# Kernel tuning notes

Measured on AMD Instinct MI355X. Metric: run time of the kernel, lower is better.

Reference implementation:

```python
import jax, jax.numpy as jnp
import numpy as np

EMB_DIM = 512
LATENT_DIM = 64
D = EMB_DIM + LATENT_DIM  # 576, kernel input per side
H1, H2 = 512, 256         # MLPKernel hidden widths
B, N, M = 2, 1024, 256


def setup_inputs() -> dict:
    key = jax.random.key(0)
    ks = jax.random.split(key, 10)
    def w(k, shape, fan_in):
        return (jax.random.normal(k, shape, dtype=jnp.float32) / np.sqrt(fan_in)).astype(jnp.float32)
    return {
        "Phi_A": jax.random.normal(ks[0], (B, N, D), dtype=jnp.float32),
        "Phi_B": jax.random.normal(ks[1], (B, M, D), dtype=jnp.float32),
        # MLPKernel params: layer1 acts on concat([a,b]) (2D -> H1); split into A/B halves
        "W1a": w(ks[2], (D, H1), 2 * D),
        "W1b": w(ks[3], (D, H1), 2 * D),
        "b1": jnp.zeros((H1,), dtype=jnp.float32),
        "W2": w(ks[4], (H1, H2), H1),
        "b2": jnp.zeros((H2,), dtype=jnp.float32),
        "W3": w(ks[5], (H2, 1), H2),
        "b3": jnp.zeros((1,), dtype=jnp.float32),
    }


def reference(Phi_A, Phi_B, W1a, W1b, b1, W2, b2, W3, b3):
    # Pairwise MLP kernel: for every (n, m), MLP(concat(Phi_A[b,n], Phi_B[b,m])).
    # First layer on concat == a@W1a + b@W1b; project each side once, then broadcast-add.
    a_proj = jnp.einsum("bnd,dh->bnh", Phi_A, W1a)          # (B, N, H1)
    b_proj = jnp.einsum("bmd,dh->bmh", Phi_B, W1b)          # (B, M, H1)
    h1 = jax.nn.relu(a_proj[:, :, None, :] + b_proj[:, None, :, :] + b1)  # (B, N, M, H1)
    h2 = jax.nn.relu(jnp.einsum("bnmh,hk->bnmk", h1, W2) + b2)            # (B, N, M, H2)
    dro = jnp.einsum("bnmk,ko->bnmo", h2, W3)[..., 0] + b3[0]             # (B, N, M)
    return dro
```

## Files before the change

kernel.cpp:

```cpp
#include <hip/hip_runtime.h>

typedef float  f4  __attribute__((ext_vector_type(4)));
typedef __bf16 bf8 __attribute__((ext_vector_type(8)));

constexpr int B_ = 2, N_ = 1024, M_ = 256, D_ = 576, H1_ = 512, H2_ = 256;

__device__ __forceinline__ void gload_lds16(const void* g, void* l) {
    __builtin_amdgcn_global_load_lds((const __attribute__((address_space(1))) void*)g,
                                     (__attribute__((address_space(3))) void*)l, 16, 0, 0);
}

__global__ __launch_bounds__(256) void k_prep(
    const float* __restrict__ W1a, const float* __restrict__ W1b, const float* __restrict__ W2,
    __bf16* __restrict__ w1aT, __bf16* __restrict__ w1bT, __bf16* __restrict__ w2T) {
    __shared__ float tl[64][65];
    int bid = blockIdx.x;
    const float* src; __bf16* dst; int R, C, t0;
    if (bid < 72)       { src = W1a; dst = w1aT; R = D_;  C = H1_; t0 = bid; }
    else if (bid < 144) { src = W1b; dst = w1bT; R = D_;  C = H1_; t0 = bid - 72; }
    else                { src = W2;  dst = w2T;  R = H1_; C = H2_; t0 = bid - 144; }
    const int tilesC = C / 64;
    const int r0 = (t0 / tilesC) * 64, c0 = (t0 % tilesC) * 64;
    const int tx = threadIdx.x & 63, ty = threadIdx.x >> 6;
    #pragma unroll
    for (int i = 0; i < 16; ++i)
        tl[ty + i * 4][tx] = src[(size_t)(r0 + ty + i * 4) * C + c0 + tx];
    __syncthreads();
    #pragma unroll
    for (int i = 0; i < 16; ++i)
        dst[(size_t)(c0 + ty + i * 4) * R + r0 + tx] = (__bf16)tl[tx][ty + i * 4];
}

__global__ __launch_bounds__(512, 2) void k_proj(
    const float* __restrict__ PhiA, const float* __restrict__ PhiB,
    const __bf16* __restrict__ w1aT, const __bf16* __restrict__ w1bT,
    const float* __restrict__ b1, float* __restrict__ aproj, __bf16* __restrict__ bprojh) {
    __shared__ __bf16 as_[2][128 * 64];
    __shared__ __bf16 ws_[2][128 * 64];
    const int t = threadIdx.x, l15 = t & 15, g = (t >> 4) & 3, wid = t >> 6;
    const int wr = wid >> 2, wc = wid & 3;
    const int by = blockIdx.x, c0 = blockIdx.y * 128;
    const bool isA = (by < 16);
    const float* srcf = isA ? PhiA : PhiB;
    const int rows0 = isA ? by * 128 : (by - 16) * 128;
    const __bf16* wt = isA ? w1aT : w1bT;

    const int ra = t >> 2, kc = (t & 3) * 16;

#define STG_A(buf, kk) do {                                                       \
    const float* ap_ = srcf + (size_t)(rows0 + ra) * D_ + (kk) + kc;              \
    f4 v0_ = *(const f4*)ap_, v1_ = *(const f4*)(ap_ + 4),                        \
       v2_ = *(const f4*)(ap_ + 8), v3_ = *(const f4*)(ap_ + 12);                 \
    bf8 h0_, h1_;                                                                 \
    _Pragma("unroll")                                                             \
    for (int j_ = 0; j_ < 4; ++j_) {                                              \
        h0_[j_] = (__bf16)v0_[j_]; h0_[4 + j_] = (__bf16)v1_[j_];                 \
        h1_[j_] = (__bf16)v2_[j_]; h1_[4 + j_] = (__bf16)v3_[j_];                 \
    }                                                                             \
    *(bf8*)((char*)(&as_[(buf)][0]) + ra * 128 + ((kc * 2) ^ ((ra & 7) << 4)))      = h0_; \
    *(bf8*)((char*)(&as_[(buf)][0]) + ra * 128 + ((kc * 2 + 16) ^ ((ra & 7) << 4))) = h1_; \
    } while (0)

#define STG_W(buf, kk) do {                                                       \
    _Pragma("unroll")                                                             \
    for (int i_ = 0; i_ < 2; ++i_) {                                              \
        int c_ = t + i_ * 512; int col_ = c_ >> 3; int gg_ = (c_ & 7) ^ (col_ & 7);\
        gload_lds16(wt + (size_t)(c0 + col_) * D_ + (kk) + gg_ * 8,               \
                    (char*)(&ws_[(buf)][0]) + c_ * 16);                           \
    } } while (0)

    f4 acc[4][2];
    #pragma unroll
    for (int fr = 0; fr < 4; ++fr)
        #pragma unroll
        for (int cf = 0; cf < 2; ++cf) acc[fr][cf] = (f4)0.0f;

    STG_A(0, 0); STG_W(0, 0);
    asm volatile("s_waitcnt vmcnt(0) lgkmcnt(0)" ::: "memory");
    __builtin_amdgcn_s_barrier();
    STG_A(1, 64); STG_W(1, 64);

    #pragma unroll 1
    for (int kt = 0; kt < 9; ++kt) {
        const int cur = kt & 1;
        #pragma unroll
        for (int ks = 0; ks < 2; ++ks) {
            bf8 av[4], bv[2];
            #pragma unroll
            for (int fr = 0; fr < 4; ++fr) {
                int row = wr * 64 + fr * 16 + l15;
                av[fr] = *(const bf8*)((const char*)(&as_[cur][0]) +
                         row * 128 + ((ks * 64 + g * 16) ^ ((row & 7) << 4)));
            }
            #pragma unroll
            for (int cf = 0; cf < 2; ++cf) {
                int col = wc * 32 + cf * 16 + l15;
                bv[cf] = *(const bf8*)((const char*)(&ws_[cur][0]) +
                         col * 128 + ((ks * 64 + g * 16) ^ ((col & 7) << 4)));
            }
            #pragma unroll
            for (int fr = 0; fr < 4; ++fr)
                #pragma unroll
                for (int cf = 0; cf < 2; ++cf)
                    acc[fr][cf] = __builtin_amdgcn_mfma_f32_16x16x32_bf16(av[fr], bv[cf], acc[fr][cf], 0, 0, 0);
        }
        if (kt == 8) break;
        asm volatile("s_waitcnt vmcnt(0) lgkmcnt(0)" ::: "memory");
        __builtin_amdgcn_s_barrier();
        if (kt < 7) { STG_A(cur, (kt + 2) * 64); STG_W(cur, (kt + 2) * 64); }
    }

    #pragma unroll
    for (int fr = 0; fr < 4; ++fr)
        #pragma unroll
        for (int cf = 0; cf < 2; ++cf) {
            int col = c0 + wc * 32 + cf * 16 + l15;
            int row = rows0 + wr * 64 + fr * 16 + g * 4;
            if (isA) {
                float bb = b1[col];
                #pragma unroll
                for (int j = 0; j < 4; ++j)
                    aproj[(size_t)(row + j) * H1_ + col] = acc[fr][cf][j] + bb;
            } else {
                #pragma unroll
                for (int j = 0; j < 4; ++j)
                    bprojh[(size_t)(row + j) * H1_ + col] = (__bf16)acc[fr][cf][j];
            }
        }
#undef STG_A
#undef STG_W
}

__global__ __launch_bounds__(512, 2) void k_main(
    const float* __restrict__ aproj, const __bf16* __restrict__ bprojh,
    const __bf16* __restrict__ w2T, const float* __restrict__ b2,
    const float* __restrict__ w3, const float* __restrict__ b3,
    float* __restrict__ outp) {
    __shared__ float  apl[16 * 512];
    __shared__ __bf16 bpl[16 * 512];
    __shared__ __bf16 w2l[2][256 * 32];
    __shared__ float  part[2][256];

    const int t = threadIdx.x, l15 = t & 15, g = (t >> 4) & 3, wid = t >> 6;
    const int wr = wid >> 1, wc = wid & 1;
    const int bid = blockIdx.x;
    const int bn0 = (bid >> 4) << 4;
    const int m0 = (bid & 15) << 4;
    const int bprow0 = ((bn0 >> 10) << 8) + m0;

    int offA[4];
    #pragma unroll
    for (int fr = 0; fr < 4; ++fr) offA[fr] = (wr * 4 + fr) * 2048 + g * 32;
    int offB[8];
    #pragma unroll
    for (int cf = 0; cf < 8; ++cf) {
        int col = wc * 128 + cf * 16 + l15;
        int cp = col >> 1, sp = (((col & 1) << 2) + g) ^ (cp & 7);
        offB[cf] = cp * 128 + sp * 16;
    }
    const int offP = l15 * 1024 + (((g ^ (l15 & 3)) | (l15 & 4)) << 4);

#define STAGE_W2M(buf, ktn) do {                                                  \
    _Pragma("unroll")                                                             \
    for (int i_ = 0; i_ < 2; ++i_) {                                              \
        int c_ = t + i_ * 512; int cp_ = c_ >> 3; int sp_ = c_ & 7;               \
        int si_ = sp_ ^ (cp_ & 7); int col_ = cp_ * 2 + (si_ >> 2);               \
        gload_lds16(w2T + (size_t)col_ * H1_ + (ktn) * 32 + (si_ & 3) * 8,        \
                    (char*)w2l + (buf) * 16384 + c_ * 16);                        \
    } } while (0)

#define STAGE_AP() do {                                                           \
    _Pragma("unroll")                                                             \
    for (int i_ = 0; i_ < 4; ++i_) {                                              \
        int c_ = t + i_ * 512;                                                    \
        gload_lds16(aproj + (size_t)(bn0 + (c_ >> 7)) * H1_ + (c_ & 127) * 4,     \
                    (char*)apl + c_ * 16);                                        \
    } } while (0)

#define STAGE_BP() do {                                                           \
    _Pragma("unroll")                                                             \
    for (int i_ = 0; i_ < 2; ++i_) {                                              \
        int c_ = t + i_ * 512; int row_ = c_ >> 6; int kc_ = (c_ & 63) ^ (row_ & 7);\
        gload_lds16(bprojh + (size_t)(bprow0 + row_) * H1_ + kc_ * 8,             \
                    (char*)bpl + c_ * 16);                                        \
    } } while (0)

    f4 acc[4][8];
    #pragma unroll
    for (int fr = 0; fr < 4; ++fr)
        #pragma unroll
        for (int cf = 0; cf < 8; ++cf) acc[fr][cf] = (f4)0.0f;

    float b2v[8], w3v[8];
    #pragma unroll
    for (int cf = 0; cf < 8; ++cf) {
        int col = wc * 128 + cf * 16 + l15;
        b2v[cf] = b2[col]; w3v[cf] = w3[col];
    }

    STAGE_AP(); STAGE_BP(); STAGE_W2M(0, 0); STAGE_W2M(1, 1);
    asm volatile("s_waitcnt vmcnt(2)" ::: "memory");
    __builtin_amdgcn_s_barrier();

    #pragma unroll
    for (int kt = 0; kt < 16; ++kt) {
        const int cur = kt & 1;
        bf8 bpv = *(const bf8*)((const char*)bpl + (offP ^ (kt * 64)));
        bf8 bv[8];
        #pragma unroll
        for (int cf = 0; cf < 8; ++cf)
            bv[cf] = *(const bf8*)((const char*)w2l + offB[cf] + cur * 16384);
        f4 a0[4], a1[4];
        #pragma unroll
        for (int fr = 0; fr < 4; ++fr) {
            a0[fr] = *(const f4*)((const char*)apl + offA[fr] + kt * 128);
            a1[fr] = *(const f4*)((const char*)apl + offA[fr] + kt * 128 + 16);
        }
        float bpf[8];
        #pragma unroll
        for (int j = 0; j < 8; ++j) bpf[j] = (float)bpv[j];
        __builtin_amdgcn_s_setprio(1);
        #pragma unroll
        for (int fr = 0; fr < 4; ++fr) {
            bf8 av;
            #pragma unroll
            for (int j = 0; j < 4; ++j) {
                av[j]     = (__bf16)fmaxf(a0[fr][j] + bpf[j],     0.0f);
                av[4 + j] = (__bf16)fmaxf(a1[fr][j] + bpf[4 + j], 0.0f);
            }
            #pragma unroll
            for (int cf = 0; cf < 8; ++cf)
                acc[fr][cf] = __builtin_amdgcn_mfma_f32_16x16x32_bf16(av, bv[cf], acc[fr][cf], 0, 0, 0);
        }
        __builtin_amdgcn_s_setprio(0);
        if (kt < 15) {
            asm volatile("" ::: "memory");
            __builtin_amdgcn_s_barrier();
            if (kt < 14) STAGE_W2M(cur, kt + 2);
            if (kt < 14) asm volatile("s_waitcnt vmcnt(2)" ::: "memory");
            else         asm volatile("s_waitcnt vmcnt(0)" ::: "memory");
            __builtin_amdgcn_s_barrier();
        }
    }

    #pragma unroll
    for (int fr = 0; fr < 4; ++fr) {
        #pragma unroll
        for (int j = 0; j < 4; ++j) {
            float s = 0.0f;
            #pragma unroll
            for (int cf = 0; cf < 8; ++cf)
                s += fmaxf(acc[fr][cf][j] + b2v[cf], 0.0f) * w3v[cf];
            s += __shfl_xor(s, 1); s += __shfl_xor(s, 2);
            s += __shfl_xor(s, 4); s += __shfl_xor(s, 8);
            if (l15 == 0) part[wc][wr * 64 + fr * 16 + g * 4 + j] = s;
        }
    }
    __syncthreads();
    if (t < 256) {
        float o = part[0][t] + part[1][t] + b3[0];
        outp[(size_t)(bn0 + (t >> 4)) * M_ + m0 + (t & 15)] = o;
    }
#undef STAGE_W2M
#undef STAGE_AP
#undef STAGE_BP
}

extern "C" void kernel_launch(void* const* d_in, const int* in_sizes, int n_in,
                              void* d_out, int out_size, void* d_ws, size_t ws_size,
                              hipStream_t stream) {
    (void)in_sizes; (void)n_in; (void)out_size; (void)ws_size;
    const float* PhiA = (const float*)d_in[0];
    const float* PhiB = (const float*)d_in[1];
    const float* W1a  = (const float*)d_in[2];
    const float* W1b  = (const float*)d_in[3];
    const float* b1   = (const float*)d_in[4];
    const float* W2   = (const float*)d_in[5];
    const float* b2   = (const float*)d_in[6];
    const float* W3   = (const float*)d_in[7];
    const float* b3   = (const float*)d_in[8];
    float* out = (float*)d_out;

    char* ws = (char*)d_ws;
    float*  aproj  = (float*)(ws);
    __bf16* bprojh = (__bf16*)(ws + 4194304);
    __bf16* w1aT   = (__bf16*)(ws + 4718592);
    __bf16* w1bT   = (__bf16*)(ws + 5308416);
    __bf16* w2T    = (__bf16*)(ws + 5898240);

    k_prep<<<176, 256, 0, stream>>>(W1a, W1b, W2, w1aT, w1bT, w2T);
    k_proj<<<dim3(20, 4), 512, 0, stream>>>(PhiA, PhiB, w1aT, w1bT, b1, aproj, bprojh);
    k_main<<<2048, 512, 0, stream>>>(aproj, bprojh, w2T, b2, W3, b3, out);
}
```

Measured before the change: 250.5 us.

## Shrink main tiles, store aproj as bf16, triple-buffer W2 with single barrier

```diff
diff --git a/kernel.cpp b/kernel.cpp
--- a/kernel.cpp
+++ b/kernel.cpp
@@ -31,18 +31,18 @@
         dst[(size_t)(c0 + ty + i * 4) * R + r0 + tx] = (__bf16)tl[tx][ty + i * 4];
 }
 
-__global__ __launch_bounds__(512, 2) void k_proj(
+__global__ __launch_bounds__(256, 2) void k_proj(
     const float* __restrict__ PhiA, const float* __restrict__ PhiB,
     const __bf16* __restrict__ w1aT, const __bf16* __restrict__ w1bT,
-    const float* __restrict__ b1, float* __restrict__ aproj, __bf16* __restrict__ bprojh) {
-    __shared__ __bf16 as_[2][128 * 64];
+    const float* __restrict__ b1, __bf16* __restrict__ aprojh, __bf16* __restrict__ bprojh) {
+    __shared__ __bf16 as_[2][64 * 64];
     __shared__ __bf16 ws_[2][128 * 64];
     const int t = threadIdx.x, l15 = t & 15, g = (t >> 4) & 3, wid = t >> 6;
-    const int wr = wid >> 2, wc = wid & 3;
+    const int wr = wid >> 1, wc = wid & 1;
     const int by = blockIdx.x, c0 = blockIdx.y * 128;
-    const bool isA = (by < 16);
+    const bool isA = (by < 32);
     const float* srcf = isA ? PhiA : PhiB;
-    const int rows0 = isA ? by * 128 : (by - 16) * 128;
+    const int rows0 = isA ? by * 64 : (by - 32) * 64;
     const __bf16* wt = isA ? w1aT : w1bT;
 
     const int ra = t >> 2, kc = (t & 3) * 16;
@@ -63,17 +63,17 @@
 
 #define STG_W(buf, kk) do {                                                       \
     _Pragma("unroll")                                                             \
-    for (int i_ = 0; i_ < 2; ++i_) {                                              \
-        int c_ = t + i_ * 512; int col_ = c_ >> 3; int gg_ = (c_ & 7) ^ (col_ & 7);\
+    for (int i_ = 0; i_ < 4; ++i_) {                                              \
+        int c_ = t + i_ * 256; int col_ = c_ >> 3; int gg_ = (c_ & 7) ^ (col_ & 7);\
         gload_lds16(wt + (size_t)(c0 + col_) * D_ + (kk) + gg_ * 8,               \
                     (char*)(&ws_[(buf)][0]) + c_ * 16);                           \
     } } while (0)
 
-    f4 acc[4][2];
-    #pragma unroll
-    for (int fr = 0; fr < 4; ++fr)
-        #pragma unroll
-        for (int cf = 0; cf < 2; ++cf) acc[fr][cf] = (f4)0.0f;
+    f4 acc[2][4];
+    #pragma unroll
+    for (int fr = 0; fr < 2; ++fr)
+        #pragma unroll
+        for (int cf = 0; cf < 4; ++cf) acc[fr][cf] = (f4)0.0f;
 
     STG_A(0, 0); STG_W(0, 0);
     asm volatile("s_waitcnt vmcnt(0) lgkmcnt(0)" ::: "memory");
@@ -85,23 +85,23 @@
         const int cur = kt & 1;
         #pragma unroll
         for (int ks = 0; ks < 2; ++ks) {
-            bf8 av[4], bv[2];
-            #pragma unroll
-            for (int fr = 0; fr < 4; ++fr) {
-                int row = wr * 64 + fr * 16 + l15;
+            bf8 av[2], bv[4];
+            #pragma unroll
+            for (int fr = 0; fr < 2; ++fr) {
+                int row = wr * 32 + fr * 16 + l15;
                 av[fr] = *(const bf8*)((const char*)(&as_[cur][0]) +
                          row * 128 + ((ks * 64 + g * 16) ^ ((row & 7) << 4)));
             }
             #pragma unroll
-            for (int cf = 0; cf < 2; ++cf) {
-                int col = wc * 32 + cf * 16 + l15;
+            for (int cf = 0; cf < 4; ++cf) {
+                int col = wc * 64 + cf * 16 + l15;
                 bv[cf] = *(const bf8*)((const char*)(&ws_[cur][0]) +
                          col * 128 + ((ks * 64 + g * 16) ^ ((col & 7) << 4)));
             }
             #pragma unroll
-            for (int fr = 0; fr < 4; ++fr)
+            for (int fr = 0; fr < 2; ++fr)
                 #pragma unroll
-                for (int cf = 0; cf < 2; ++cf)
+                for (int cf = 0; cf < 4; ++cf)
                     acc[fr][cf] = __builtin_amdgcn_mfma_f32_16x16x32_bf16(av[fr], bv[cf], acc[fr][cf], 0, 0, 0);
         }
         if (kt == 8) break;
@@ -111,16 +111,16 @@
     }
 
     #pragma unroll
-    for (int fr = 0; fr < 4; ++fr)
-        #pragma unroll
-        for (int cf = 0; cf < 2; ++cf) {
-            int col = c0 + wc * 32 + cf * 16 + l15;
-            int row = rows0 + wr * 64 + fr * 16 + g * 4;
+    for (int fr = 0; fr < 2; ++fr)
+        #pragma unroll
+        for (int cf = 0; cf < 4; ++cf) {
+            int col = c0 + wc * 64 + cf * 16 + l15;
+            int row = rows0 + wr * 32 + fr * 16 + g * 4;
             if (isA) {
                 float bb = b1[col];
                 #pragma unroll
                 for (int j = 0; j < 4; ++j)
-                    aproj[(size_t)(row + j) * H1_ + col] = acc[fr][cf][j] + bb;
+                    aprojh[(size_t)(row + j) * H1_ + col] = (__bf16)(acc[fr][cf][j] + bb);
             } else {
                 #pragma unroll
                 for (int j = 0; j < 4; ++j)
@@ -131,26 +131,26 @@
 #undef STG_W
 }
 
-__global__ __launch_bounds__(512, 2) void k_main(
-    const float* __restrict__ aproj, const __bf16* __restrict__ bprojh,
+__global__ __launch_bounds__(256, 2) void k_main(
+    const __bf16* __restrict__ aprojh, const __bf16* __restrict__ bprojh,
     const __bf16* __restrict__ w2T, const float* __restrict__ b2,
     const float* __restrict__ w3, const float* __restrict__ b3,
     float* __restrict__ outp) {
-    __shared__ float  apl[16 * 512];
+    __shared__ __bf16 apl[8 * 512];
     __shared__ __bf16 bpl[16 * 512];
-    __shared__ __bf16 w2l[2][256 * 32];
-    __shared__ float  part[2][256];
+    __shared__ __bf16 w2l[3][256 * 32];
+    __shared__ float  part[2][128];
 
     const int t = threadIdx.x, l15 = t & 15, g = (t >> 4) & 3, wid = t >> 6;
     const int wr = wid >> 1, wc = wid & 1;
     const int bid = blockIdx.x;
-    const int bn0 = (bid >> 4) << 4;
-    const int m0 = (bid & 15) << 4;
+    const int bn0 = (bid >> 4) * 8;
+    const int m0 = (bid & 15) * 16;
     const int bprow0 = ((bn0 >> 10) << 8) + m0;
 
-    int offA[4];
-    #pragma unroll
-    for (int fr = 0; fr < 4; ++fr) offA[fr] = (wr * 4 + fr) * 2048 + g * 32;
+    int apA[4];
+    #pragma unroll
+    for (int fr = 0; fr < 4; ++fr) apA[fr] = (wr * 4 + fr) * 1024 + g * 16;
     int offB[8];
     #pragma unroll
     for (int cf = 0; cf < 8; ++cf) {
@@ -160,27 +160,27 @@
     }
     const int offP = l15 * 1024 + (((g ^ (l15 & 3)) | (l15 & 4)) << 4);
 
-#define STAGE_W2M(buf, ktn) do {                                                  \
-    _Pragma("unroll")                                                             \
-    for (int i_ = 0; i_ < 2; ++i_) {                                              \
-        int c_ = t + i_ * 512; int cp_ = c_ >> 3; int sp_ = c_ & 7;               \
+#define STAGE_W2M(stoff, ktn) do {                                                \
+    _Pragma("unroll")                                                             \
+    for (int i_ = 0; i_ < 4; ++i_) {                                              \
+        int c_ = t + i_ * 256; int cp_ = c_ >> 3; int sp_ = c_ & 7;               \
         int si_ = sp_ ^ (cp_ & 7); int col_ = cp_ * 2 + (si_ >> 2);               \
         gload_lds16(w2T + (size_t)col_ * H1_ + (ktn) * 32 + (si_ & 3) * 8,        \
-                    (char*)w2l + (buf) * 16384 + c_ * 16);                        \
+                    (char*)w2l + (stoff) + c_ * 16);                              \
     } } while (0)
 
 #define STAGE_AP() do {                                                           \
     _Pragma("unroll")                                                             \
+    for (int i_ = 0; i_ < 2; ++i_) {                                              \
+        int c_ = t + i_ * 256;                                                    \
+        gload_lds16(aprojh + (size_t)(bn0 + (c_ >> 6)) * H1_ + (c_ & 63) * 8,     \
+                    (char*)apl + c_ * 16);                                        \
+    } } while (0)
+
+#define STAGE_BP() do {                                                           \
+    _Pragma("unroll")                                                             \
     for (int i_ = 0; i_ < 4; ++i_) {                                              \
-        int c_ = t + i_ * 512;                                                    \
-        gload_lds16(aproj + (size_t)(bn0 + (c_ >> 7)) * H1_ + (c_ & 127) * 4,     \
-                    (char*)apl + c_ * 16);                                        \
-    } } while (0)
-
-#define STAGE_BP() do {                                                           \
-    _Pragma("unroll")                                                             \
-    for (int i_ = 0; i_ < 2; ++i_) {                                              \
-        int c_ = t + i_ * 512; int row_ = c_ >> 6; int kc_ = (c_ & 63) ^ (row_ & 7);\
+        int c_ = t + i_ * 256; int row_ = c_ >> 6; int kc_ = (c_ & 63) ^ (row_ & 7);\
         gload_lds16(bprojh + (size_t)(bprow0 + row_) * H1_ + kc_ * 8,             \
                     (char*)bpl + c_ * 16);                                        \
     } } while (0)
@@ -190,6 +190,48 @@
     for (int fr = 0; fr < 4; ++fr)
         #pragma unroll
         for (int cf = 0; cf < 8; ++cf) acc[fr][cf] = (f4)0.0f;
+
+    STAGE_AP(); STAGE_BP(); STAGE_W2M(0, 0);
+    STAGE_W2M(16384, 1);
+    asm volatile("s_waitcnt vmcnt(4)" ::: "memory");
+    __builtin_amdgcn_s_barrier();
+
+    int rdoff = 0, stoff = 32768;
+    #pragma unroll 1
+    for (int kt = 0; kt < 16; ++kt) {
+        if (kt < 14) STAGE_W2M(stoff, kt + 2);
+        const char* wsl = (const char*)w2l + rdoff;
+        bf8 bv[8];
+        #pragma unroll
+        for (int cf = 0; cf < 8; ++cf) bv[cf] = *(const bf8*)(wsl + offB[cf]);
+        bf8 bpv = *(const bf8*)((const char*)bpl + (offP ^ (kt * 64)));
+        bf8 apv[4];
+        #pragma unroll
+        for (int fr = 0; fr < 4; ++fr)
+            apv[fr] = *(const bf8*)((const char*)apl + apA[fr] + kt * 64);
+        float bpf[8];
+        #pragma unroll
+        for (int j = 0; j < 8; ++j) bpf[j] = (float)bpv[j];
+        __builtin_amdgcn_s_setprio(1);
+        #pragma unroll
+        for (int fr = 0; fr < 4; ++fr) {
+            bf8 av;
+            #pragma unroll
+            for (int j = 0; j < 4; ++j) {
+                av[j]     = (__bf16)fmaxf((float)apv[fr][j]     + bpf[j],     0.0f);
+                av[4 + j] = (__bf16)fmaxf((float)apv[fr][4 + j] + bpf[4 + j], 0.0f);
+            }
+            #pragma unroll
+            for (int cf = 0; cf < 8; ++cf)
+                acc[fr][cf] = __builtin_amdgcn_mfma_f32_16x16x32_bf16(av, bv[cf], acc[fr][cf], 0, 0, 0);
+        }
+        __builtin_amdgcn_s_setprio(0);
+        if (kt < 14)       asm volatile("s_waitcnt vmcnt(4)" ::: "memory");
+        else if (kt == 14) asm volatile("s_waitcnt vmcnt(0)" ::: "memory");
+        if (kt < 15) __builtin_amdgcn_s_barrier();
+        rdoff = (rdoff == 32768) ? 0 : rdoff + 16384;
+        stoff = (stoff == 32768) ? 0 : stoff + 16384;
+    }
 
     float b2v[8], w3v[8];
     #pragma unroll
@@ -197,52 +239,6 @@
         int col = wc * 128 + cf * 16 + l15;
         b2v[cf] = b2[col]; w3v[cf] = w3[col];
     }
-
-    STAGE_AP(); STAGE_BP(); STAGE_W2M(0, 0); STAGE_W2M(1, 1);
-    asm volatile("s_waitcnt vmcnt(2)" ::: "memory");
-    __builtin_amdgcn_s_barrier();
-
-    #pragma unroll
-    for (int kt = 0; kt < 16; ++kt) {
-        const int cur = kt & 1;
-        bf8 bpv = *(const bf8*)((const char*)bpl + (offP ^ (kt * 64)));
-        bf8 bv[8];
-        #pragma unroll
-        for (int cf = 0; cf < 8; ++cf)
-            bv[cf] = *(const bf8*)((const char*)w2l + offB[cf] + cur * 16384);
-        f4 a0[4], a1[4];
-        #pragma unroll
-        for (int fr = 0; fr < 4; ++fr) {
-            a0[fr] = *(const f4*)((const char*)apl + offA[fr] + kt * 128);
-            a1[fr] = *(const f4*)((const char*)apl + offA[fr] + kt * 128 + 16);
-        }
-        float bpf[8];
-        #pragma unroll
-        for (int j = 0; j < 8; ++j) bpf[j] = (float)bpv[j];
-        __builtin_amdgcn_s_setprio(1);
-        #pragma unroll
-        for (int fr = 0; fr < 4; ++fr) {
-            bf8 av;
-            #pragma unroll
-            for (int j = 0; j < 4; ++j) {
-                av[j]     = (__bf16)fmaxf(a0[fr][j] + bpf[j],     0.0f);
-                av[4 + j] = (__bf16)fmaxf(a1[fr][j] + bpf[4 + j], 0.0f);
-            }
-            #pragma unroll
-            for (int cf = 0; cf < 8; ++cf)
-                acc[fr][cf] = __builtin_amdgcn_mfma_f32_16x16x32_bf16(av, bv[cf], acc[fr][cf], 0, 0, 0);
-        }
-        __builtin_amdgcn_s_setprio(0);
-        if (kt < 15) {
-            asm volatile("" ::: "memory");
-            __builtin_amdgcn_s_barrier();
-            if (kt < 14) STAGE_W2M(cur, kt + 2);
-            if (kt < 14) asm volatile("s_waitcnt vmcnt(2)" ::: "memory");
-            else         asm volatile("s_waitcnt vmcnt(0)" ::: "memory");
-            __builtin_amdgcn_s_barrier();
-        }
-    }
-
     #pragma unroll
     for (int fr = 0; fr < 4; ++fr) {
         #pragma unroll
@@ -253,11 +249,11 @@
                 s += fmaxf(acc[fr][cf][j] + b2v[cf], 0.0f) * w3v[cf];
             s += __shfl_xor(s, 1); s += __shfl_xor(s, 2);
             s += __shfl_xor(s, 4); s += __shfl_xor(s, 8);
-            if (l15 == 0) part[wc][wr * 64 + fr * 16 + g * 4 + j] = s;
+            if (l15 == 0) part[wc][(wr * 4 + fr) * 16 + g * 4 + j] = s;
         }
     }
     __syncthreads();
-    if (t < 256) {
+    if (t < 128) {
         float o = part[0][t] + part[1][t] + b3[0];
         outp[(size_t)(bn0 + (t >> 4)) * M_ + m0 + (t & 15)] = o;
     }
@@ -282,13 +278,13 @@
     float* out = (float*)d_out;
 
     char* ws = (char*)d_ws;
-    float*  aproj  = (float*)(ws);
-    __bf16* bprojh = (__bf16*)(ws + 4194304);
-    __bf16* w1aT   = (__bf16*)(ws + 4718592);
-    __bf16* w1bT   = (__bf16*)(ws + 5308416);
-    __bf16* w2T    = (__bf16*)(ws + 5898240);
+    __bf16* aprojh = (__bf16*)(ws);
+    __bf16* bprojh = (__bf16*)(ws + 2097152);
+    __bf16* w1aT   = (__bf16*)(ws + 2621440);
+    __bf16* w1bT   = (__bf16*)(ws + 3211264);
+    __bf16* w2T    = (__bf16*)(ws + 3801088);
 
     k_prep<<<176, 256, 0, stream>>>(W1a, W1b, W2, w1aT, w1bT, w2T);
-    k_proj<<<dim3(20, 4), 512, 0, stream>>>(PhiA, PhiB, w1aT, w1bT, b1, aproj, bprojh);
-    k_main<<<2048, 512, 0, stream>>>(aproj, bprojh, w2T, b2, W3, b3, out);
-}
+    k_proj<<<dim3(40, 4), 256, 0, stream>>>(PhiA, PhiB, w1aT, w1bT, b1, aprojh, bprojh);
+    k_main<<<4096, 256, 0, stream>>>(aprojh, bprojh, w2T, b2, W3, b3, out);
+}
```

Measured after the change: 250.3 us. No clear change (-0.1%).
